# Kernel optimization log

Measured on AMD Instinct MI355X. Metric: run time of the kernel, lower is better.

Reference implementation:

```python
import jax, jax.numpy as jnp
import numpy as np

N = 50000
E = 800000
D = 64


def _linear_params(key, d, bias=True):
    kw, kb = jax.random.split(key)
    s = 1.0 / np.sqrt(d)
    W = jax.random.uniform(kw, (d, d), jnp.float32, -s, s)
    if bias:
        b = jax.random.uniform(kb, (d,), jnp.float32, -s, s)
        return W, b
    return W


def setup_inputs() -> dict:
    key = jax.random.key(0)
    ks = jax.random.split(key, 12)
    x_src = jax.random.normal(ks[0], (N, D), jnp.float32)
    x_tgt = jax.random.normal(ks[1], (N, D), jnp.float32)
    t_src = jax.random.normal(ks[2], (N, D), jnp.float32)
    t_tgt = jax.random.normal(ks[3], (N, D), jnp.float32)
    edge_index = jax.random.randint(ks[4], (2, E), 0, N, jnp.int64)
    W_x = _linear_params(ks[5], D, bias=False)
    W_t = _linear_params(ks[6], D, bias=False)
    Ka_W, Ka_b = _linear_params(ks[7], D)
    Qa_W, Qa_b = _linear_params(ks[8], D)
    Kb_W, Kb_b = _linear_params(ks[9], D)
    Qb_W, Qb_b = _linear_params(ks[10], D)
    return dict(x_src=x_src, x_tgt=x_tgt, t_src=t_src, t_tgt=t_tgt,
                edge_index=edge_index, W_x=W_x, W_t=W_t,
                Ka_W=Ka_W, Ka_b=Ka_b, Qa_W=Qa_W, Qa_b=Qa_b,
                Kb_W=Kb_W, Kb_b=Kb_b, Qb_W=Qb_W, Qb_b=Qb_b)


def _segment_softmax(scores, seg, num_segments):
    # numerically stable softmax over edges sharing the same destination node
    m = jax.ops.segment_max(scores, seg, num_segments=num_segments)
    ex = jnp.exp(scores - m[seg])
    denom = jax.ops.segment_sum(ex, seg, num_segments=num_segments)
    return ex / denom[seg]


def reference(x_src, x_tgt, t_src, t_tgt, edge_index,
              W_x, W_t, Ka_W, Ka_b, Qa_W, Qa_b, Kb_W, Kb_b, Qb_W, Qb_b):
    row, col = edge_index[0], edge_index[1]
    n = x_tgt.shape[0]
    d = x_src.shape[-1]
    scale = 1.0 / jnp.sqrt(jnp.float32(d))

    # project on nodes first (cheaper than per-edge), then gather per edge
    q_alpha = (t_tgt @ Qa_W.T + Qa_b)[row]   # [E, D]
    k_alpha = (t_src @ Ka_W.T + Ka_b)[col]
    alpha = _segment_softmax(jnp.sum(q_alpha * k_alpha, -1) * scale, row, n)

    q_beta = (x_tgt @ Qb_W.T + Qb_b)[row]
    k_beta = (x_src @ Kb_W.T + Kb_b)[col]
    beta = _segment_softmax(jnp.sum(q_beta * k_beta, -1) * scale, row, n)

    msg_t = alpha[:, None] * (t_src @ W_t.T)[col]  # [E, D]
    msg_x = beta[:, None] * (x_src @ W_x.T)[col]

    out_x = jax.ops.segment_sum(msg_x, row, num_segments=n)
    out_t = jax.ops.segment_sum(msg_t, row, num_segments=n)
    return out_x, out_t
```

## Files before the change

### kernel.cpp

```cpp
#include <hip/hip_runtime.h>
#include <math.h>


#define D 64
#define NINF -3.0e38f
#define CHUNK 4096
typedef unsigned short ushortT;
typedef unsigned long long ull;
typedef __attribute__((ext_vector_type(8))) short bf16x8;
typedef __attribute__((ext_vector_type(4))) float f32x4;

__device__ __forceinline__ float b2f_lo(unsigned u) {
  return __uint_as_float(u << 16);
}
__device__ __forceinline__ float b2f_hi(unsigned u) {
  return __uint_as_float(u & 0xffff0000u);
}
__device__ __forceinline__ ushortT f2b(float f) {
  unsigned u = __float_as_uint(f);
  u += 0x7fffu + ((u >> 16) & 1u);
  return (ushortT)(u >> 16);
}
__device__ __forceinline__ bf16x8 pack8(float4 v0, float4 v1) {
  bf16x8 r;
  r[0] = (short)f2b(v0.x); r[1] = (short)f2b(v0.y);
  r[2] = (short)f2b(v0.z); r[3] = (short)f2b(v0.w);
  r[4] = (short)f2b(v1.x); r[5] = (short)f2b(v1.y);
  r[6] = (short)f2b(v1.z); r[7] = (short)f2b(v1.w);
  return r;
}

__device__ __forceinline__ bool wave_is64(const ull* __restrict__ ei, ull nNodes) {
  ull v = ei[threadIdx.x & 63];
  return __ballot(v >= nNodes) == 0ull;
}

__global__ __launch_bounds__(256) void pack_hist(
    const void* __restrict__ ei, int* __restrict__ hist, int E, int N) {
  __shared__ int h[256];
  const int t = threadIdx.x;
  h[t] = 0;
  __syncthreads();
  const bool is64 = wave_is64((const ull*)ei, (ull)N);
  const int base = blockIdx.x * CHUNK + t;
  if (is64) {
    const long long* p = (const long long*)ei;
#pragma unroll 4
    for (int k = 0; k < 16; ++k) {
      int e = base + k * 256;
      if (e < E) atomicAdd(&h[((unsigned)(int)p[e]) >> 8], 1);
    }
  } else {
    const int* p = (const int*)ei;
#pragma unroll 4
    for (int k = 0; k < 16; ++k) {
      int e = base + k * 256;
      if (e < E) atomicAdd(&h[((unsigned)p[e]) >> 8], 1);
    }
  }
  __syncthreads();
  hist[blockIdx.x * 256 + t] = h[t];
}

__global__ __launch_bounds__(256) void scat_proj(
    const void* __restrict__ ei, const int* __restrict__ hist,
    int* __restrict__ bucketStart, int* __restrict__ offs,
    unsigned* __restrict__ bucketed, int E,
    const float* __restrict__ t_tgt, const float* __restrict__ x_tgt,
    const float* __restrict__ t_src, const float* __restrict__ x_src,
    const float* __restrict__ QaW, const float* __restrict__ Qab_,
    const float* __restrict__ QbW, const float* __restrict__ Qbb,
    const float* __restrict__ KaW, const float* __restrict__ Kab_,
    const float* __restrict__ Wt,
    const float* __restrict__ KbW, const float* __restrict__ Kbb,
    const float* __restrict__ Wx,
    float* __restrict__ qab, ushortT* __restrict__ kab, ushortT* __restrict__ vtx,
    int N, int bpj, int scatBlocks) {
  const int tid = threadIdx.x;

  if (blockIdx.x < scatBlocks) {
    __shared__ int baseA[256];
    __shared__ int cnt[256];
    __shared__ int lofs[256];
    __shared__ int cnt2[256];
    __shared__ int scT[256];
    __shared__ unsigned lpack[CHUNK];
    const int b = blockIdx.x;
    int pre = 0, tot = 0;
    for (int i = 0; i < scatBlocks; ++i) {
      int v = hist[i * 256 + tid];
      if (i < b) pre += v;
      tot += v;
    }
    scT[tid] = tot;
    __syncthreads();
    for (int off = 1; off < 256; off <<= 1) {
      int add = (tid >= off) ? scT[tid - off] : 0;
      __syncthreads();
      scT[tid] += add;
      __syncthreads();
    }
    const int bstart = scT[tid] - tot;
    baseA[tid] = bstart + pre;
    cnt[tid] = 0;
    cnt2[tid] = 0;
    if (b == 0) {
      bucketStart[tid] = bstart;
      if (tid == 0) {
        bucketStart[256] = E;
        offs[N] = E;
      }
    }
    __syncthreads();
    const bool is64 = wave_is64((const ull*)ei, (ull)N);
    int r[16], c[16];
    const int base = b * CHUNK + tid;
    if (is64) {
      const long long* p = (const long long*)ei;
#pragma unroll
      for (int k = 0; k < 16; ++k) {
        int e = base + k * 256;
        r[k] = (e < E) ? (int)p[e] : -1;
        c[k] = (e < E) ? (int)p[(long long)E + e] : 0;
      }
    } else {
      const int* p = (const int*)ei;
#pragma unroll
      for (int k = 0; k < 16; ++k) {
        int e = base + k * 256;
        r[k] = (e < E) ? p[e] : -1;
        c[k] = (e < E) ? p[E + e] : 0;
      }
    }
#pragma unroll
    for (int k = 0; k < 16; ++k)
      if (r[k] >= 0) atomicAdd(&cnt[r[k] >> 8], 1);
    __syncthreads();
    const int cv = cnt[tid];
    scT[tid] = cv;
    __syncthreads();
    for (int off = 1; off < 256; off <<= 1) {
      int add = (tid >= off) ? scT[tid - off] : 0;
      __syncthreads();
      scT[tid] += add;
      __syncthreads();
    }
    lofs[tid] = scT[tid] - cv;
    __syncthreads();
#pragma unroll
    for (int k = 0; k < 16; ++k) {
      if (r[k] >= 0) {
        int bin = r[k] >> 8;
        int kk = atomicAdd(&cnt2[bin], 1);
        lpack[lofs[bin] + kk] = ((unsigned)r[k] << 16) | (unsigned)c[k];
      }
    }
    __syncthreads();
    const int rem = E - b * CHUNK;
    const int nblk = rem < CHUNK ? rem : CHUNK;
    for (int i = tid; i < nblk; i += 256) {
      unsigned v = lpack[i];
      int bin = v >> 24;
      bucketed[baseA[bin] + (i - lofs[bin])] = v;
    }
    return;
  }

  const int tile = blockIdx.x - scatBlocks;
  const int job = tile / bpj;
  const int jb = tile % bpj;
  const float *X, *W0, *B0, *W1 = nullptr;
  switch (job) {
    case 0: X = t_tgt; W0 = QaW; B0 = Qab_; break;
    case 1: X = x_tgt; W0 = QbW; B0 = Qbb; break;
    case 2: X = t_src; W0 = KaW; B0 = Kab_; W1 = Wt; break;
    default: X = x_src; W0 = KbW; B0 = Kbb; W1 = Wx; break;
  }
  const bool dual = (job >= 2);
  const int half = (job & 1) ? 64 : 0;
  const int base = jb * 128;

  const int lane = tid & 63;
  const int wid = tid >> 6;
  const int m16 = lane & 15;
  const int quad = lane >> 4;

  f32x4 acc0[2][4], acc1[2][4];
#pragma unroll
  for (int mt = 0; mt < 2; ++mt)
#pragma unroll
    for (int nt = 0; nt < 4; ++nt) {
      acc0[mt][nt] = (f32x4){0.f, 0.f, 0.f, 0.f};
      acc1[mt][nt] = (f32x4){0.f, 0.f, 0.f, 0.f};
    }

#pragma unroll
  for (int ko = 0; ko < 2; ++ko) {
    const int koff = ko * 32 + quad * 8;
    bf16x8 a[2];
#pragma unroll
    for (int mt = 0; mt < 2; ++mt) {
      const int gnode = base + wid * 32 + mt * 16 + m16;
      float4 v0 = make_float4(0.f, 0.f, 0.f, 0.f), v1 = v0;
      if (gnode < N) {
        const float* p = X + (size_t)gnode * D + koff;
        v0 = *(const float4*)p;
        v1 = *(const float4*)(p + 4);
      }
      a[mt] = pack8(v0, v1);
    }
#pragma unroll
    for (int nt = 0; nt < 4; ++nt) {
      const float* pw = W0 + (nt * 16 + m16) * D + koff;
      bf16x8 bfr = pack8(*(const float4*)pw, *(const float4*)(pw + 4));
#pragma unroll
      for (int mt = 0; mt < 2; ++mt)
        acc0[mt][nt] = __builtin_amdgcn_mfma_f32_16x16x32_bf16(
            a[mt], bfr, acc0[mt][nt], 0, 0, 0);
    }
    if (dual) {
#pragma unroll
      for (int nt = 0; nt < 4; ++nt) {
        const float* pw = W1 + (nt * 16 + m16) * D + koff;
        bf16x8 bfr = pack8(*(const float4*)pw, *(const float4*)(pw + 4));
#pragma unroll
        for (int mt = 0; mt < 2; ++mt)
          acc1[mt][nt] = __builtin_amdgcn_mfma_f32_16x16x32_bf16(
              a[mt], bfr, acc1[mt][nt], 0, 0, 0);
      }
    }
  }

  float bias[4];
#pragma unroll
  for (int nt = 0; nt < 4; ++nt) bias[nt] = B0[nt * 16 + m16];
#pragma unroll
  for (int mt = 0; mt < 2; ++mt) {
#pragma unroll
    for (int reg = 0; reg < 4; ++reg) {
      int node = base + wid * 32 + mt * 16 + quad * 4 + reg;
      if (node < N) {
        if (!dual) {
          float* dst = qab + (size_t)node * 128 + half;
#pragma unroll
          for (int nt = 0; nt < 4; ++nt)
            dst[nt * 16 + m16] = acc0[mt][nt][reg] + bias[nt];
        } else {
          ushortT* dk = kab + (size_t)node * 128 + half;
          ushortT* dv = vtx + (size_t)node * 128 + half;
#pragma unroll
          for (int nt = 0; nt < 4; ++nt) {
            dk[nt * 16 + m16] = f2b(acc0[mt][nt][reg] + bias[nt]);
            dv[nt * 16 + m16] = f2b(acc1[mt][nt][reg]);
          }
        }
      }
    }
  }
}

__global__ __launch_bounds__(256) void build_csr(
    const unsigned* __restrict__ bucketed, const int* __restrict__ bucketStart,
    int* __restrict__ offs, ushortT* __restrict__ ecol, int N) {
  __shared__ int cnt[256], sc[256], cnt2[256];
  __shared__ ushortT lcol[8192];
  const int t = threadIdx.x;
  const int b = blockIdx.x;
  const int start = bucketStart[b];
  int nb = bucketStart[b + 1] - start;
  if (nb > 8192) nb = 8192;
  cnt[t] = 0;
  cnt2[t] = 0;
  __syncthreads();
  for (int i = t; i < nb; i += 256)
    atomicAdd(&cnt[(bucketed[start + i] >> 16) & 255], 1);
  __syncthreads();
  const int c = cnt[t];
  sc[t] = c;
  __syncthreads();
  for (int off = 1; off < 256; off <<= 1) {
    int add = (t >= off) ? sc[t - off] : 0;
    __syncthreads();
    sc[t] += add;
    __syncthreads();
  }
  const int loffs_t = sc[t] - c;
  sc[t] = loffs_t;
  const int row = b * 256 + t;
  if (row < N) offs[row] = start + loffs_t;
  __syncthreads();
  for (int i = t; i < nb; i += 256) {
    unsigned v = bucketed[start + i];
    int r = (v >> 16) & 255;
    int pos = sc[r] + atomicAdd(&cnt2[r], 1);
    lcol[pos] = (ushortT)(v & 0xFFFFu);
  }
  __syncthreads();
  for (int i = t; i < nb; i += 256) ecol[start + i] = lcol[i];
}

__global__ __launch_bounds__(256) void node_attn(
    const float* __restrict__ qab, const ushortT* __restrict__ kab,
    const ushortT* __restrict__ vtx,
    const int* __restrict__ offs, const ushortT* __restrict__ ecol,
    float* __restrict__ out_x, float* __restrict__ out_t, int nNodes) {
  const int lane = threadIdx.x & 63;
  const int sub = lane >> 4;
  const int sl = lane & 15;
  const int gw = (blockIdx.x * blockDim.x + threadIdx.x) >> 6;
  const int nw = (gridDim.x * blockDim.x) >> 6;
  const float scale = 0.125f;

  for (int n = gw; n < nNodes; n += nw) {
    const int s = offs[n];
    const int dg = offs[n + 1] - s;
    const size_t nb = (size_t)n * D;
    if (dg == 0) {
      out_t[nb + lane] = 0.f;
      out_x[nb + lane] = 0.f;
      continue;
    }
    const float4 q0 = *(const float4*)(qab + (size_t)n * 128 + sl * 8);
    const float4 q1 = *(const float4*)(qab + (size_t)n * 128 + sl * 8 + 4);

    float m = NINF, d = 0.f;
    float acc[8];
#pragma unroll
    for (int j = 0; j < 8; ++j) acc[j] = 0.f;

    for (int i = 0; i < dg; i += 8) {
      const int i0 = i + sub;
      const int i1 = i + 4 + sub;
      const bool a0 = i0 < dg, a1 = i1 < dg;
      const int c0 = (int)ecol[s + (a0 ? i0 : 0)];
      const int c1 = (int)ecol[s + (a1 ? i1 : 0)];
      const uint4 k0 = *(const uint4*)(kab + (size_t)c0 * 128 + sl * 8);
      const uint4 v0 = *(const uint4*)(vtx + (size_t)c0 * 128 + sl * 8);
      const uint4 k1 = *(const uint4*)(kab + (size_t)c1 * 128 + sl * 8);
      const uint4 v1 = *(const uint4*)(vtx + (size_t)c1 * 128 + sl * 8);

      {
        float t = q0.x * b2f_lo(k0.x);
        t = fmaf(q0.y, b2f_hi(k0.x), t);
        t = fmaf(q0.z, b2f_lo(k0.y), t);
        t = fmaf(q0.w, b2f_hi(k0.y), t);
        t = fmaf(q1.x, b2f_lo(k0.z), t);
        t = fmaf(q1.y, b2f_hi(k0.z), t);
        t = fmaf(q1.z, b2f_lo(k0.w), t);
        t = fmaf(q1.w, b2f_hi(k0.w), t);
#pragma unroll
        for (int off = 1; off < 8; off <<= 1) t += __shfl_xor(t, off);
        const float sc = a0 ? t * scale : NINF;
        const float mN = fmaxf(m, sc);
        const float f = __expf(m - mN);
        const float w = a0 ? __expf(sc - mN) : 0.f;
        d = d * f + w;
        acc[0] = fmaf(acc[0], f, w * b2f_lo(v0.x));
        acc[1] = fmaf(acc[1], f, w * b2f_hi(v0.x));
        acc[2] = fmaf(acc[2], f, w * b2f_lo(v0.y));
        acc[3] = fmaf(acc[3], f, w * b2f_hi(v0.y));
        acc[4] = fmaf(acc[4], f, w * b2f_lo(v0.z));
        acc[5] = fmaf(acc[5], f, w * b2f_hi(v0.z));
        acc[6] = fmaf(acc[6], f, w * b2f_lo(v0.w));
        acc[7] = fmaf(acc[7], f, w * b2f_hi(v0.w));
        m = mN;
      }
      {
        float t = q0.x * b2f_lo(k1.x);
        t = fmaf(q0.y, b2f_hi(k1.x), t);
        t = fmaf(q0.z, b2f_lo(k1.y), t);
        t = fmaf(q0.w, b2f_hi(k1.y), t);
        t = fmaf(q1.x, b2f_lo(k1.z), t);
        t = fmaf(q1.y, b2f_hi(k1.z), t);
        t = fmaf(q1.z, b2f_lo(k1.w), t);
        t = fmaf(q1.w, b2f_hi(k1.w), t);
#pragma unroll
        for (int off = 1; off < 8; off <<= 1) t += __shfl_xor(t, off);
        const float sc = a1 ? t * scale : NINF;
        const float mN = fmaxf(m, sc);
        const float f = __expf(m - mN);
        const float w = a1 ? __expf(sc - mN) : 0.f;
        d = d * f + w;
        acc[0] = fmaf(acc[0], f, w * b2f_lo(v1.x));
        acc[1] = fmaf(acc[1], f, w * b2f_hi(v1.x));
        acc[2] = fmaf(acc[2], f, w * b2f_lo(v1.y));
        acc[3] = fmaf(acc[3], f, w * b2f_hi(v1.y));
        acc[4] = fmaf(acc[4], f, w * b2f_lo(v1.z));
        acc[5] = fmaf(acc[5], f, w * b2f_hi(v1.z));
        acc[6] = fmaf(acc[6], f, w * b2f_lo(v1.w));
        acc[7] = fmaf(acc[7], f, w * b2f_hi(v1.w));
        m = mN;
      }
    }

    float mg = m;
#pragma unroll
    for (int off = 16; off < 64; off <<= 1) mg = fmaxf(mg, __shfl_xor(mg, off));
    const float fg = __expf(m - mg);
    d *= fg;
#pragma unroll
    for (int j = 0; j < 8; ++j) acc[j] *= fg;
#pragma unroll
    for (int off = 16; off < 64; off <<= 1) {
      d += __shfl_xor(d, off);
#pragma unroll
      for (int j = 0; j < 8; ++j) acc[j] += __shfl_xor(acc[j], off);
    }
    const float inv = 1.0f / d;
    if (sub == 0) {
      float4 o0, o1;
      o0.x = acc[0] * inv; o0.y = acc[1] * inv;
      o0.z = acc[2] * inv; o0.w = acc[3] * inv;
      o1.x = acc[4] * inv; o1.y = acc[5] * inv;
      o1.z = acc[6] * inv; o1.w = acc[7] * inv;
      float* dst = (sl < 8) ? (out_t + nb + sl * 8) : (out_x + nb + (sl - 8) * 8);
      *(float4*)dst = o0;
      *(float4*)(dst + 4) = o1;
    }
  }
}

extern "C" void kernel_launch(void* const* d_in, const int* in_sizes, int n_in,
                              void* d_out, int out_size, void* d_ws, size_t ws_size,
                              hipStream_t stream) {
  const float* x_src = (const float*)d_in[0];
  const float* x_tgt = (const float*)d_in[1];
  const float* t_src = (const float*)d_in[2];
  const float* t_tgt = (const float*)d_in[3];
  const void* edge_index = d_in[4];
  const float* W_x = (const float*)d_in[5];
  const float* W_t = (const float*)d_in[6];
  const float* Ka_W = (const float*)d_in[7];
  const float* Ka_b = (const float*)d_in[8];
  const float* Qa_W = (const float*)d_in[9];
  const float* Qa_b = (const float*)d_in[10];
  const float* Kb_W = (const float*)d_in[11];
  const float* Kb_b = (const float*)d_in[12];
  const float* Qb_W = (const float*)d_in[13];
  const float* Qb_b = (const float*)d_in[14];

  const int N = in_sizes[0] / D;
  const int E = in_sizes[4] / 2;

  char* ws = (char*)d_ws;
  size_t ofs = 0;
  auto carve = [&](size_t bytes) {
    size_t p = ofs;
    ofs += (bytes + 255) & ~(size_t)255;
    return p;
  };
  float* qab = (float*)(ws + carve((size_t)N * 128 * 4));
  ushortT* kab = (ushortT*)(ws + carve((size_t)N * 128 * 2));
  ushortT* vtx = (ushortT*)(ws + carve((size_t)N * 128 * 2));
  unsigned* bucketed = (unsigned*)(ws + carve((size_t)E * 4));
  ushortT* ecol = (ushortT*)(ws + carve((size_t)E * 2));
  const int nBlocks = (E + CHUNK - 1) / CHUNK;
  int* hist = (int*)(ws + carve((size_t)nBlocks * 256 * 4));
  int* bucketStart = (int*)(ws + carve(257 * 4));
  int* offs = (int*)(ws + carve(((size_t)N + 1) * 4));
  (void)ws_size;

  float* out_x = (float*)d_out;
  float* out_t = out_x + (size_t)N * D;

  const int bpj = (N + 127) / 128;
  const int projBlocks = 4 * bpj;

  pack_hist<<<nBlocks, 256, 0, stream>>>(edge_index, hist, E, N);
  scat_proj<<<nBlocks + projBlocks, 256, 0, stream>>>(
      edge_index, hist, bucketStart, offs, bucketed, E,
      t_tgt, x_tgt, t_src, x_src,
      Qa_W, Qa_b, Qb_W, Qb_b,
      Ka_W, Ka_b, W_t,
      Kb_W, Kb_b, W_x,
      qab, kab, vtx, N, bpj, nBlocks);
  build_csr<<<256, 256, 0, stream>>>(bucketed, bucketStart, offs, ecol, N);
  node_attn<<<(N + 3) / 4, 256, 0, stream>>>(qab, kab, vtx, offs, ecol,
                                             out_x, out_t, N);
}
```

Before: 228.5 us.

## Precompute histogram scans in dedicated kernels and split node_attn launch

Moves the per-block prefix computation over the bucket histogram out of scat_proj into two small scan kernels: a per-bin exclusive scan across blocks and a single-block scan of the bin totals. Each scatter block previously looped over all blocks' histograms and redid a 256-wide scan, which was redundant O(nBlocks) work per block. The node attention kernel is also split into two launches covering each half of the nodes. This adds two extra kernel launches plus a second node_attn launch, with their launch and serialization overhead.

```diff
diff --git a/kernel.cpp b/kernel.cpp
--- a/kernel.cpp
+++ b/kernel.cpp
@@ -62,10 +62,48 @@
   hist[blockIdx.x * 256 + t] = h[t];
 }
 
+__global__ __launch_bounds__(256) void scan_bins(
+    int* __restrict__ hist, int* __restrict__ binTotal, int nBlocks) {
+  __shared__ int sc[256];
+  const int t = threadIdx.x;
+  const int bin = blockIdx.x;
+  const int v = (t < nBlocks) ? hist[t * 256 + bin] : 0;
+  sc[t] = v;
+  __syncthreads();
+  for (int off = 1; off < 256; off <<= 1) {
+    int add = (t >= off) ? sc[t - off] : 0;
+    __syncthreads();
+    sc[t] += add;
+    __syncthreads();
+  }
+  if (t < nBlocks) hist[t * 256 + bin] = sc[t] - v;
+  if (t == 255) binTotal[bin] = sc[255];
+}
+
+__global__ __launch_bounds__(256) void scan_base(
+    const int* __restrict__ binTotal, int* __restrict__ bucketStart,
+    int* __restrict__ offs, int E, int N) {
+  __shared__ int sc[256];
+  const int t = threadIdx.x;
+  const int v = binTotal[t];
+  sc[t] = v;
+  __syncthreads();
+  for (int off = 1; off < 256; off <<= 1) {
+    int add = (t >= off) ? sc[t - off] : 0;
+    __syncthreads();
+    sc[t] += add;
+    __syncthreads();
+  }
+  bucketStart[t] = sc[t] - v;
+  if (t == 0) {
+    bucketStart[256] = E;
+    offs[N] = E;
+  }
+}
+
 __global__ __launch_bounds__(256) void scat_proj(
     const void* __restrict__ ei, const int* __restrict__ hist,
-    int* __restrict__ bucketStart, int* __restrict__ offs,
-    unsigned* __restrict__ bucketed, int E,
+    const int* __restrict__ bucketStart, unsigned* __restrict__ bucketed, int E,
     const float* __restrict__ t_tgt, const float* __restrict__ x_tgt,
     const float* __restrict__ t_src, const float* __restrict__ x_src,
     const float* __restrict__ QaW, const float* __restrict__ Qab_,
@@ -86,31 +124,9 @@
     __shared__ int scT[256];
     __shared__ unsigned lpack[CHUNK];
     const int b = blockIdx.x;
-    int pre = 0, tot = 0;
-    for (int i = 0; i < scatBlocks; ++i) {
-      int v = hist[i * 256 + tid];
-      if (i < b) pre += v;
-      tot += v;
-    }
-    scT[tid] = tot;
-    __syncthreads();
-    for (int off = 1; off < 256; off <<= 1) {
-      int add = (tid >= off) ? scT[tid - off] : 0;
-      __syncthreads();
-      scT[tid] += add;
-      __syncthreads();
-    }
-    const int bstart = scT[tid] - tot;
-    baseA[tid] = bstart + pre;
+    baseA[tid] = bucketStart[tid] + hist[b * 256 + tid];
     cnt[tid] = 0;
     cnt2[tid] = 0;
-    if (b == 0) {
-      bucketStart[tid] = bstart;
-      if (tid == 0) {
-        bucketStart[256] = E;
-        offs[N] = E;
-      }
-    }
     __syncthreads();
     const bool is64 = wave_is64((const ull*)ei, (ull)N);
     int r[16], c[16];
@@ -303,7 +319,7 @@
     const float* __restrict__ qab, const ushortT* __restrict__ kab,
     const ushortT* __restrict__ vtx,
     const int* __restrict__ offs, const ushortT* __restrict__ ecol,
-    float* __restrict__ out_x, float* __restrict__ out_t, int nNodes) {
+    float* __restrict__ out_x, float* __restrict__ out_t, int n0, int n1) {
   const int lane = threadIdx.x & 63;
   const int sub = lane >> 4;
   const int sl = lane & 15;
@@ -311,7 +327,7 @@
   const int nw = (gridDim.x * blockDim.x) >> 6;
   const float scale = 0.125f;
 
-  for (int n = gw; n < nNodes; n += nw) {
+  for (int n = n0 + gw; n < n1; n += nw) {
     const int s = offs[n];
     const int dg = offs[n + 1] - s;
     const size_t nb = (size_t)n * D;
@@ -456,6 +472,7 @@
   ushortT* ecol = (ushortT*)(ws + carve((size_t)E * 2));
   const int nBlocks = (E + CHUNK - 1) / CHUNK;
   int* hist = (int*)(ws + carve((size_t)nBlocks * 256 * 4));
+  int* binTotal = (int*)(ws + carve(256 * 4));
   int* bucketStart = (int*)(ws + carve(257 * 4));
   int* offs = (int*)(ws + carve(((size_t)N + 1) * 4));
   (void)ws_size;
@@ -465,16 +482,21 @@
 
   const int bpj = (N + 127) / 128;
   const int projBlocks = 4 * bpj;
+  const int nHalf = N / 2;
 
   pack_hist<<<nBlocks, 256, 0, stream>>>(edge_index, hist, E, N);
+  scan_bins<<<256, 256, 0, stream>>>(hist, binTotal, nBlocks);
+  scan_base<<<1, 256, 0, stream>>>(binTotal, bucketStart, offs, E, N);
   scat_proj<<<nBlocks + projBlocks, 256, 0, stream>>>(
-      edge_index, hist, bucketStart, offs, bucketed, E,
+      edge_index, hist, bucketStart, bucketed, E,
       t_tgt, x_tgt, t_src, x_src,
       Qa_W, Qa_b, Qb_W, Qb_b,
       Ka_W, Ka_b, W_t,
       Kb_W, Kb_b, W_x,
       qab, kab, vtx, N, bpj, nBlocks);
   build_csr<<<256, 256, 0, stream>>>(bucketed, bucketStart, offs, ecol, N);
-  node_attn<<<(N + 3) / 4, 256, 0, stream>>>(qab, kab, vtx, offs, ecol,
-                                             out_x, out_t, N);
-}
+  node_attn<<<(nHalf + 3) / 4, 256, 0, stream>>>(qab, kab, vtx, offs, ecol,
+                                                 out_x, out_t, 0, nHalf);
+  node_attn<<<(N - nHalf + 3) / 4, 256, 0, stream>>>(qab, kab, vtx, offs, ecol,
+                                                     out_x, out_t, nHalf, N);
+}
```

After: 231.8 us. Within noise of the previous version (+1.4%).
